# Optimization experiments

Measured on AMD Instinct MI355X. Metric: run time of the kernel, lower is better.

The kernel has to match this reference:

```python
import jax, jax.numpy as jnp
import numpy as np

DIM = 256
HEADS = 4
HEAD_DIM = DIM // HEADS  # 64
SCALE = (DIM / HEADS) ** -0.5
EPS = 1e-5


def layer_norm(x, g, b):
    mu = jnp.mean(x, axis=-1, keepdims=True)
    var = jnp.mean(jnp.square(x - mu), axis=-1, keepdims=True)
    return (x - mu) * jax.lax.rsqrt(var + EPS) * g + b


def setup_inputs() -> dict:
    key = jax.random.key(0)
    ks = jax.random.split(key, 8)
    B, N, C = 2, 64 * 64, DIM
    H = 4 * DIM  # mlp hidden
    s = lambda fan: 1.0 / np.sqrt(fan)
    return {
        "x": jax.random.normal(ks[0], (B, N, C), jnp.float32),
        "w_qkv": jax.random.normal(ks[1], (C, 3 * C), jnp.float32) * s(C),
        "w_ao": jax.random.normal(ks[2], (C, C), jnp.float32) * s(C),
        "b_ao": jnp.zeros((C,), jnp.float32),
        "g_ao": jnp.ones((C,), jnp.float32),
        "be_ao": jnp.zeros((C,), jnp.float32),
        "g1": jnp.ones((C,), jnp.float32),
        "be1": jnp.zeros((C,), jnp.float32),
        "w_fc1": jax.random.normal(ks[3], (C, H), jnp.float32) * s(C),
        "b_fc1": jnp.zeros((H,), jnp.float32),
        "w_fc2": jax.random.normal(ks[4], (H, C), jnp.float32) * s(H),
        "b_fc2": jnp.zeros((C,), jnp.float32),
        "g2": jnp.ones((C,), jnp.float32),
        "be2": jnp.zeros((C,), jnp.float32),
    }


def reference(x, w_qkv, w_ao, b_ao, g_ao, be_ao, g1, be1,
              w_fc1, b_fc1, w_fc2, b_fc2, g2, be2):
    b, n, c = x.shape
    shortcut = x

    # --- LinearAttention ---
    qkv = x @ w_qkv  # [b, n, 3c]
    qkv = qkv.reshape(b, n, 3, HEADS, HEAD_DIM).transpose(2, 0, 3, 1, 4)  # [3,b,h,n,d]
    q, k, v = qkv[0], qkv[1], qkv[2]
    k = jax.nn.softmax(k, axis=-2)  # softmax over sequence dim
    q = q * SCALE
    context = jnp.einsum('bhid,bhjd->bhij', k, v)   # [b,h,n,n]
    out = jnp.einsum('bhij,bhid->bhjd', context, q)  # [b,h,n,d]
    out = out.reshape(b, n, c)  # faithful to torch reshape (no transpose)
    attn_out = layer_norm(out @ w_ao + b_ao, g_ao, be_ao)

    # --- block residuals ---
    h = shortcut + layer_norm(attn_out, g1, be1)
    mlp = jax.nn.gelu(h @ w_fc1 + b_fc1) @ w_fc2 + b_fc2
    h = h + layer_norm(mlp, g2, be2)
    return shortcut + h
```

## Files before the change

kernel.cpp:

```cpp
#include <hip/hip_runtime.h>

typedef __attribute__((ext_vector_type(8))) short short8;
typedef __attribute__((ext_vector_type(4))) float f32x4;

#define EPSF 1e-5f
#define NSEQ 4096
#define R_TOT 8192

__device__ __forceinline__ float bf2f(unsigned short u){
  union { unsigned int i; float f; } v; v.i = ((unsigned int)u) << 16; return v.f;
}
__device__ __forceinline__ unsigned short f2bf(float f){
  union { float f; unsigned int i; } v; v.f = f;
  unsigned int u = v.i;
  u += 0x7FFFu + ((u >> 16) & 1u);
  return (unsigned short)(u >> 16);
}
__device__ __forceinline__ float wsum(float v){
  #pragma unroll
  for (int o = 32; o > 0; o >>= 1) v += __shfl_xor(v, o, 64);
  return v;
}
__device__ __forceinline__ float gelu_tanh(float x){
  float y = 0.7978845608028654f * (x + 0.044715f * x * x * x);
  float e = __expf(2.0f * y);
  float th = 1.0f - 2.0f / (e + 1.0f);
  return 0.5f * x * (1.0f + th);
}
__device__ __forceinline__ void gload_lds16(const unsigned short* g, unsigned short* l){
  __builtin_amdgcn_global_load_lds(
      (const __attribute__((address_space(1))) unsigned int*)g,
      (__attribute__((address_space(3))) unsigned int*)l, 16, 0, 0);
}

__global__ void k_prep(const float* __restrict__ x, unsigned short* __restrict__ xbf,
                       const float* __restrict__ w_qkv, const float* __restrict__ w_ao,
                       const float* __restrict__ w_fc1, const float* __restrict__ w_fc2,
                       unsigned short* __restrict__ oq, unsigned short* __restrict__ oa,
                       unsigned short* __restrict__ o1, unsigned short* __restrict__ o2)
{
  int bid = blockIdx.x;
  const int t = threadIdx.x;
  if (bid < 2048){
    int i = (bid * 256 + t) * 4;
    float4 v = *(const float4*)(x + i);
    ushort4 o;
    o.x = f2bf(v.x); o.y = f2bf(v.y); o.z = f2bf(v.z); o.w = f2bf(v.w);
    *(ushort4*)(xbf + i) = o;
    return;
  }
  bid -= 2048;
  const float* in; unsigned short* out; int rows, cols, tid;
  if (bid < 48)      { in = w_qkv; out = oq; rows = 256;  cols = 768;  tid = bid; }
  else if (bid < 64) { in = w_ao;  out = oa; rows = 256;  cols = 256;  tid = bid - 48; }
  else if (bid < 128){ in = w_fc1; out = o1; rows = 256;  cols = 1024; tid = bid - 64; }
  else               { in = w_fc2; out = o2; rows = 1024; cols = 256;  tid = bid - 128; }
  const int tC = cols >> 6;
  const int r0 = (tid / tC) * 64, c0 = (tid % tC) * 64;
  __shared__ float tile[64][68];
  const int i = t >> 4, j4 = (t & 15) * 4;
  #pragma unroll
  for (int p = 0; p < 4; p++){
    float4 v = *(const float4*)(in + (size_t)(r0 + i + p * 16) * cols + c0 + j4);
    tile[i + p * 16][j4 + 0] = v.x; tile[i + p * 16][j4 + 1] = v.y;
    tile[i + p * 16][j4 + 2] = v.z; tile[i + p * 16][j4 + 3] = v.w;
  }
  __syncthreads();
  #pragma unroll
  for (int p = 0; p < 4; p++){
    int ci = i + p * 16;
    ushort4 o;
    o.x = f2bf(tile[j4 + 0][ci]); o.y = f2bf(tile[j4 + 1][ci]);
    o.z = f2bf(tile[j4 + 2][ci]); o.w = f2bf(tile[j4 + 3][ci]);
    *(ushort4*)(out + (size_t)(c0 + ci) * rows + r0 + j4) = o;
  }
}

template<int BM, int BN, bool HAS_BIAS, bool DO_GELU, bool OUT_BF16>
__global__ __launch_bounds__(256) void k_gemm(const unsigned short* __restrict__ A,
                       const unsigned short* __restrict__ BT,
                       const float* __restrict__ bias,
                       float* __restrict__ Cf,
                       unsigned short* __restrict__ Cb,
                       int M, int N, int K)
{
  constexpr int BK = 64;
  constexpr int FM = BM / 32, FN = BN / 32;
  __shared__ unsigned short As[2][BM * BK];
  __shared__ unsigned short Bs[2][BN * BK];
  const int t  = threadIdx.x;
  const int l  = t & 63;
  const int w  = t >> 6;
  const int wm = w >> 1, wn = w & 1;
  const int lr = l & 15, kq = l >> 4;
  const int m0 = blockIdx.y * BM, n0 = blockIdx.x * BN;

  f32x4 acc[FM][FN];
  #pragma unroll
  for (int i = 0; i < FM; i++)
    #pragma unroll
    for (int j = 0; j < FN; j++) acc[i][j] = (f32x4){0.f, 0.f, 0.f, 0.f};

  const int crow = l >> 3, ccolE = (l & 7) * 8;
  const int nk = K / BK;

  auto stage = [&](int s, int bsel){
    #pragma unroll
    for (int c = w; c < BM / 8; c += 4)
      gload_lds16(A  + (size_t)(m0 + c * 8 + crow) * K + s * BK + ccolE, &As[bsel][c * 512]);
    #pragma unroll
    for (int c = w; c < BN / 8; c += 4)
      gload_lds16(BT + (size_t)(n0 + c * 8 + crow) * K + s * BK + ccolE, &Bs[bsel][c * 512]);
  };

  stage(0, 0);
  __syncthreads();
  for (int s = 0; s < nk; ++s){
    const int cur = s & 1;
    if (s + 1 < nk) stage(s + 1, cur ^ 1);
    #pragma unroll
    for (int kk = 0; kk < BK; kk += 32){
      short8 af[FM], bfr[FN];
      #pragma unroll
      for (int i = 0; i < FM; i++)
        af[i]  = *(const short8*)&As[cur][(wm * (BM / 2) + i * 16 + lr) * 64 + kk + kq * 8];
      #pragma unroll
      for (int j = 0; j < FN; j++)
        bfr[j] = *(const short8*)&Bs[cur][(wn * (BN / 2) + j * 16 + lr) * 64 + kk + kq * 8];
      #pragma unroll
      for (int i = 0; i < FM; i++)
        #pragma unroll
        for (int j = 0; j < FN; j++)
          acc[i][j] = __builtin_amdgcn_mfma_f32_16x16x32_bf16(af[i], bfr[j], acc[i][j], 0, 0, 0);
    }
    __syncthreads();
  }

  const int row0 = m0 + wm * (BM / 2);
  const int col0 = n0 + wn * (BN / 2);
  #pragma unroll
  for (int i = 0; i < FM; i++){
    #pragma unroll
    for (int j = 0; j < FN; j++){
      #pragma unroll
      for (int r = 0; r < 4; r++){
        int row = row0 + i * 16 + kq * 4 + r;
        int col = col0 + j * 16 + lr;
        float v = acc[i][j][r];
        if (HAS_BIAS) v += bias[col];
        if (DO_GELU)  v = gelu_tanh(v);
        if (OUT_BF16) Cb[(size_t)row * N + col] = f2bf(v);
        else          Cf[(size_t)row * N + col] = v;
      }
    }
  }
}

#define NPAD 72
__global__ __launch_bounds__(256) void k_msum(const unsigned short* __restrict__ qkv,
                                              float* __restrict__ Spart,
                                              float* __restrict__ dsum_part)
{
  __shared__ unsigned short kT[64 * NPAD];
  __shared__ unsigned short qT[80 * NPAD];
  const int t = threadIdx.x;
  const int sl = blockIdx.x;
  const int bh = blockIdx.y;
  const int b = bh >> 2, h = bh & 3;
  const int e4 = (t & 15) * 4;
  const int col = (t >> 4) * 4;
  const int w4 = t >> 6, lr = t & 15, kq = (t >> 4) & 3;

  f32x4 acc[5];
  #pragma unroll
  for (int j = 0; j < 5; ++j) acc[j] = (f32x4){0.f, 0.f, 0.f, 0.f};

  for (int ch = 0; ch < 4; ++ch){
    int n = sl * 256 + ch * 64 + col;
    const unsigned short* rp = qkv + (size_t)(b * NSEQ + n) * 768 + h * 64 + e4;
    ushort4 q0 = *(const ushort4*)(rp);
    ushort4 q1 = *(const ushort4*)(rp + 768);
    ushort4 q2 = *(const ushort4*)(rp + 1536);
    ushort4 q3 = *(const ushort4*)(rp + 2304);
    ushort4 k0 = *(const ushort4*)(rp + 256);
    ushort4 k1 = *(const ushort4*)(rp + 1024);
    ushort4 k2 = *(const ushort4*)(rp + 1792);
    ushort4 k3 = *(const ushort4*)(rp + 2560);
    if (ch) __syncthreads();
    ushort4 w;
    w.x = q0.x; w.y = q1.x; w.z = q2.x; w.w = q3.x; *(ushort4*)&qT[(e4+0)*NPAD + col] = w;
    w.x = q0.y; w.y = q1.y; w.z = q2.y; w.w = q3.y; *(ushort4*)&qT[(e4+1)*NPAD + col] = w;
    w.x = q0.z; w.y = q1.z; w.z = q2.z; w.w = q3.z; *(ushort4*)&qT[(e4+2)*NPAD + col] = w;
    w.x = q0.w; w.y = q1.w; w.z = q2.w; w.w = q3.w; *(ushort4*)&qT[(e4+3)*NPAD + col] = w;
    w.x = f2bf(__expf(bf2f(k0.x))); w.y = f2bf(__expf(bf2f(k1.x)));
    w.z = f2bf(__expf(bf2f(k2.x))); w.w = f2bf(__expf(bf2f(k3.x)));
    *(ushort4*)&kT[(e4+0)*NPAD + col] = w;
    w.x = f2bf(__expf(bf2f(k0.y))); w.y = f2bf(__expf(bf2f(k1.y)));
    w.z = f2bf(__expf(bf2f(k2.y))); w.w = f2bf(__expf(bf2f(k3.y)));
    *(ushort4*)&kT[(e4+1)*NPAD + col] = w;
    w.x = f2bf(__expf(bf2f(k0.z))); w.y = f2bf(__expf(bf2f(k1.z)));
    w.z = f2bf(__expf(bf2f(k2.z))); w.w = f2bf(__expf(bf2f(k3.z)));
    *(ushort4*)&kT[(e4+2)*NPAD + col] = w;
    w.x = f2bf(__expf(bf2f(k0.w))); w.y = f2bf(__expf(bf2f(k1.w)));
    w.z = f2bf(__expf(bf2f(k2.w))); w.w = f2bf(__expf(bf2f(k3.w)));
    *(ushort4*)&kT[(e4+3)*NPAD + col] = w;
    if (ch == 0 && t < 16){
      ushort4 ones; ones.x = 0x3F80; ones.y = 0x3F80; ones.z = 0x3F80; ones.w = 0x3F80;
      *(ushort4*)&qT[64 * NPAD + t * 4] = ones;
    }
    __syncthreads();
    #pragma unroll
    for (int ks = 0; ks < 2; ++ks){
      int nc = ks * 32 + kq * 8;
      short8 af = *(const short8*)&kT[(w4 * 16 + lr) * NPAD + nc];
      #pragma unroll
      for (int j = 0; j < 5; ++j){
        short8 bf = *(const short8*)&qT[(j * 16 + lr) * NPAD + nc];
        acc[j] = __builtin_amdgcn_mfma_f32_16x16x32_bf16(af, bf, acc[j], 0, 0, 0);
      }
    }
  }
  float* sp = Spart + ((size_t)sl * 8 + bh) * 4096;
  #pragma unroll
  for (int j = 0; j < 4; ++j)
    #pragma unroll
    for (int r = 0; r < 4; ++r)
      sp[(w4 * 16 + kq * 4 + r) * 64 + j * 16 + lr] = acc[j][r];
  if (lr == 0){
    float* dp = dsum_part + (sl * 8 + bh) * 64;
    #pragma unroll
    for (int r = 0; r < 4; ++r) dp[w4 * 16 + kq * 4 + r] = acc[4][r];
  }
}

__global__ __launch_bounds__(256) void k_projvm_dln(
    const unsigned short* __restrict__ qkv,
    const float* __restrict__ Spart, const float* __restrict__ dsum_part,
    const unsigned short* __restrict__ waoT,
    const float* __restrict__ bias, const float* __restrict__ x,
    const float* __restrict__ g_ao, const float* __restrict__ be_ao,
    const float* __restrict__ g1, const float* __restrict__ be1,
    unsigned short* __restrict__ hbf, float* __restrict__ sxh)
{
  __shared__ __align__(16) char smem[16896 + 16384 + 8192 + 65536];
  unsigned short* As   = (unsigned short*)smem;
  unsigned short* vlds = (unsigned short*)(smem + 16896);
  unsigned short* mt   = (unsigned short*)(smem + 16896 + 16384);
  unsigned short* Bs0  = (unsigned short*)(smem + 41472);
  float*          yt   = (float*)(smem + 41472);

  const int t = threadIdx.x, l = t & 63, w = t >> 6;
  const int lr = l & 15, kq = l >> 4;
  const int m0 = blockIdx.x * 32;
  const int b = m0 >> 12, h = (m0 >> 10) & 3;
  const int bh = b * 4 + h;
  const int n0 = (m0 & 1023) * 4;
  const int crow = l >> 3, ccolE = (l & 7) * 8;

  const unsigned short* vbase = qkv + (size_t)(b * NSEQ + n0) * 768 + 512 + h * 64;
  #pragma unroll
  for (int c = w; c < 16; c += 4)
    gload_lds16(vbase + (size_t)(c * 8 + crow) * 768 + ccolE, vlds + c * 512);
  #pragma unroll
  for (int c = w; c < 32; c += 4)
    gload_lds16(waoT + (size_t)(c * 8 + crow) * 256 + ccolE, Bs0 + c * 512);
  {
    int e = t >> 2, d0 = (t & 3) * 16;
    float dn = 0.f;
    #pragma unroll
    for (int sl = 0; sl < 16; ++sl) dn += dsum_part[(sl * 8 + bh) * 64 + e];
    float rdn = 0.125f / dn;
    #pragma unroll
    for (int i = 0; i < 16; i += 4){
      float4 mv = {0.f, 0.f, 0.f, 0.f};
      #pragma unroll
      for (int sl = 0; sl < 16; ++sl){
        float4 p = *(const float4*)(Spart + ((size_t)sl * 8 + bh) * 4096 + e * 64 + d0 + i);
        mv.x += p.x; mv.y += p.y; mv.z += p.z; mv.w += p.w;
      }
      mt[(d0 + i + 0) * 64 + e] = f2bf(mv.x * rdn);
      mt[(d0 + i + 1) * 64 + e] = f2bf(mv.y * rdn);
      mt[(d0 + i + 2) * 64 + e] = f2bf(mv.z * rdn);
      mt[(d0 + i + 3) * 64 + e] = f2bf(mv.w * rdn);
    }
  }
  __syncthreads();
  {
    f32x4 vacc[2][4];
    #pragma unroll
    for (int i = 0; i < 2; i++)
      #pragma unroll
      for (int j = 0; j < 4; j++) vacc[i][j] = (f32x4){0.f, 0.f, 0.f, 0.f};
    #pragma unroll
    for (int kk = 0; kk < 64; kk += 32){
      short8 vf[2], mf[4];
      #pragma unroll
      for (int i = 0; i < 2; i++)
        vf[i] = *(const short8*)&vlds[((w * 2 + i) * 16 + lr) * 64 + kk + kq * 8];
      #pragma unroll
      for (int j = 0; j < 4; j++)
        mf[j] = *(const short8*)&mt[(j * 16 + lr) * 64 + kk + kq * 8];
      #pragma unroll
      for (int i = 0; i < 2; i++)
        #pragma unroll
        for (int j = 0; j < 4; j++)
          vacc[i][j] = __builtin_amdgcn_mfma_f32_16x16x32_bf16(vf[i], mf[j], vacc[i][j], 0, 0, 0);
    }
    #pragma unroll
    for (int i = 0; i < 2; i++)
      #pragma unroll
      for (int j = 0; j < 4; j++)
        #pragma unroll
        for (int r = 0; r < 4; r++)
          As[((w * 2 + i) * 4 + kq) * 264 + r * 64 + j * 16 + lr] = f2bf(vacc[i][j][r]);
  }
  __syncthreads();
  f32x4 acc[2][4];
  #pragma unroll
  for (int i = 0; i < 2; i++)
    #pragma unroll
    for (int j = 0; j < 4; j++) acc[i][j] = (f32x4){0.f, 0.f, 0.f, 0.f};
  for (int s = 0; s < 4; ++s){
    const int cur = s & 1;
    if (s + 1 < 4){
      unsigned short* bnxt = Bs0 + (cur ^ 1) * 16384;
      #pragma unroll
      for (int c = w; c < 32; c += 4)
        gload_lds16(waoT + (size_t)(c * 8 + crow) * 256 + (s + 1) * 64 + ccolE,
                    bnxt + c * 512);
    }
    const unsigned short* bcur = Bs0 + cur * 16384;
    #pragma unroll
    for (int kk = 0; kk < 64; kk += 32){
      short8 af[2], bfr[4];
      #pragma unroll
      for (int i = 0; i < 2; i++)
        af[i] = *(const short8*)&As[(i * 16 + lr) * 264 + s * 64 + kk + kq * 8];
      #pragma unroll
      for (int j = 0; j < 4; j++)
        bfr[j] = *(const short8*)&bcur[(w * 64 + j * 16 + lr) * 64 + kk + kq * 8];
      #pragma unroll
      for (int i = 0; i < 2; i++)
        #pragma unroll
        for (int j = 0; j < 4; j++)
          acc[i][j] = __builtin_amdgcn_mfma_f32_16x16x32_bf16(af[i], bfr[j], acc[i][j], 0, 0, 0);
    }
    __syncthreads();
  }
  #pragma unroll
  for (int i = 0; i < 2; i++)
    #pragma unroll
    for (int j = 0; j < 4; j++){
      float bv = bias[w * 64 + j * 16 + lr];
      #pragma unroll
      for (int r = 0; r < 4; r++)
        yt[(i * 16 + kq * 4 + r) * 260 + w * 64 + j * 16 + lr] = acc[i][j][r] + bv;
    }
  __syncthreads();
  const int gl = t & 63;
  #pragma unroll
  for (int rp = 0; rp < 8; rp++){
    int row = rp * 4 + (t >> 6);
    float4 v = *(const float4*)(yt + row * 260 + gl * 4);
    float mu = wsum(v.x + v.y + v.z + v.w) * 0.00390625f;
    float dx = v.x - mu, dy = v.y - mu, dz = v.z - mu, dw = v.w - mu;
    float rstd = rsqrtf(wsum(dx*dx + dy*dy + dz*dz + dw*dw) * 0.00390625f + EPSF);
    float4 ga = *(const float4*)(g_ao + gl * 4);
    float4 ba = *(const float4*)(be_ao + gl * 4);
    float zx = dx * rstd * ga.x + ba.x, zy = dy * rstd * ga.y + ba.y;
    float zz = dz * rstd * ga.z + ba.z, zw = dw * rstd * ga.w + ba.w;
    float mu2 = wsum(zx + zy + zz + zw) * 0.00390625f;
    float ex = zx - mu2, ey = zy - mu2, ez = zz - mu2, ew = zw - mu2;
    float rstd2 = rsqrtf(wsum(ex*ex + ey*ey + ez*ez + ew*ew) * 0.00390625f + EPSF);
    float4 gb = *(const float4*)(g1 + gl * 4);
    float4 bb = *(const float4*)(be1 + gl * 4);
    size_t off = (size_t)(m0 + row) * 256 + gl * 4;
    float4 xr = *(const float4*)(x + off);
    float hx = xr.x + ex * rstd2 * gb.x + bb.x;
    float hy = xr.y + ey * rstd2 * gb.y + bb.y;
    float hz = xr.z + ez * rstd2 * gb.z + bb.z;
    float hw = xr.w + ew * rstd2 * gb.w + bb.w;
    ushort4 hb; hb.x = f2bf(hx); hb.y = f2bf(hy); hb.z = f2bf(hz); hb.w = f2bf(hw);
    *(ushort4*)(hbf + off) = hb;
    float4 sv = {xr.x + hx, xr.y + hy, xr.z + hz, xr.w + hw};
    *(float4*)(sxh + off) = sv;
  }
}

__global__ __launch_bounds__(256) void k_fc2_ln(
    const unsigned short* __restrict__ A, const unsigned short* __restrict__ BT,
    const float* __restrict__ bias, const float* __restrict__ sxh,
    const float* __restrict__ g2, const float* __restrict__ be2,
    float* __restrict__ out)
{
  constexpr int K = 1024;
  __shared__ __align__(16) char smem[8192 + 65536];
  unsigned short* As0 = (unsigned short*)smem;
  unsigned short* Bs0 = (unsigned short*)(smem + 8192);
  float* yt = (float*)(smem + 8192);
  const int t = threadIdx.x, l = t & 63, w = t >> 6;
  const int lr = l & 15, kq = l >> 4;
  const int m0 = blockIdx.x * 32;
  const int crow = l >> 3, ccolE = (l & 7) * 8;
  f32x4 acc[2][4];
  #pragma unroll
  for (int i = 0; i < 2; i++)
    #pragma unroll
    for (int j = 0; j < 4; j++) acc[i][j] = (f32x4){0.f, 0.f, 0.f, 0.f};

  auto stage = [&](int s, int bsel){
    gload_lds16(A + (size_t)(m0 + w * 8 + crow) * K + s * 64 + ccolE,
                As0 + bsel * 2048 + w * 512);
    unsigned short* bdst = Bs0 + bsel * 16384;
    #pragma unroll
    for (int c = w; c < 32; c += 4)
      gload_lds16(BT + (size_t)(c * 8 + crow) * K + s * 64 + ccolE, bdst + c * 512);
  };

  stage(0, 0);
  __syncthreads();
  for (int s = 0; s < 16; ++s){
    const int cur = s & 1;
    if (s + 1 < 16) stage(s + 1, cur ^ 1);
    const unsigned short* acur = As0 + cur * 2048;
    const unsigned short* bcur = Bs0 + cur * 16384;
    #pragma unroll
    for (int kk = 0; kk < 64; kk += 32){
      short8 af[2], bfr[4];
      #pragma unroll
      for (int i = 0; i < 2; i++)
        af[i] = *(const short8*)&acur[(i * 16 + lr) * 64 + kk + kq * 8];
      #pragma unroll
      for (int j = 0; j < 4; j++)
        bfr[j] = *(const short8*)&bcur[(w * 64 + j * 16 + lr) * 64 + kk + kq * 8];
      #pragma unroll
      for (int i = 0; i < 2; i++)
        #pragma unroll
        for (int j = 0; j < 4; j++)
          acc[i][j] = __builtin_amdgcn_mfma_f32_16x16x32_bf16(af[i], bfr[j], acc[i][j], 0, 0, 0);
    }
    __syncthreads();
  }
  #pragma unroll
  for (int i = 0; i < 2; i++)
    #pragma unroll
    for (int j = 0; j < 4; j++){
      float bv = bias[w * 64 + j * 16 + lr];
      #pragma unroll
      for (int r = 0; r < 4; r++)
        yt[(i * 16 + kq * 4 + r) * 260 + w * 64 + j * 16 + lr] = acc[i][j][r] + bv;
    }
  __syncthreads();
  const int gl = t & 63;
  #pragma unroll
  for (int rp = 0; rp < 8; rp++){
    int row = rp * 4 + (t >> 6);
    float4 v = *(const float4*)(yt + row * 260 + gl * 4);
    float mu = wsum(v.x + v.y + v.z + v.w) * 0.00390625f;
    float dx = v.x - mu, dy = v.y - mu, dz = v.z - mu, dw = v.w - mu;
    float rstd = rsqrtf(wsum(dx*dx + dy*dy + dz*dz + dw*dw) * 0.00390625f + EPSF);
    float4 g = *(const float4*)(g2 + gl * 4);
    float4 be = *(const float4*)(be2 + gl * 4);
    size_t off = (size_t)(m0 + row) * 256 + gl * 4;
    float4 sv = *(const float4*)(sxh + off);
    float4 o;
    o.x = sv.x + dx * rstd * g.x + be.x;
    o.y = sv.y + dy * rstd * g.y + be.y;
    o.z = sv.z + dz * rstd * g.z + be.z;
    o.w = sv.w + dw * rstd * g.w + be.w;
    *(float4*)(out + off) = o;
  }
}

extern "C" void kernel_launch(void* const* d_in, const int* in_sizes, int n_in,
                              void* d_out, int out_size, void* d_ws, size_t ws_size,
                              hipStream_t stream)
{
  const float* x     = (const float*)d_in[0];
  const float* w_qkv = (const float*)d_in[1];
  const float* w_ao  = (const float*)d_in[2];
  const float* b_ao  = (const float*)d_in[3];
  const float* g_ao  = (const float*)d_in[4];
  const float* be_ao = (const float*)d_in[5];
  const float* g1    = (const float*)d_in[6];
  const float* be1   = (const float*)d_in[7];
  const float* w_fc1 = (const float*)d_in[8];
  const float* b_fc1 = (const float*)d_in[9];
  const float* w_fc2 = (const float*)d_in[10];
  const float* b_fc2 = (const float*)d_in[11];
  const float* g2    = (const float*)d_in[12];
  const float* be2   = (const float*)d_in[13];
  float* out = (float*)d_out;
  char* ws = (char*)d_ws;

  unsigned short* qkv   = (unsigned short*)(ws + 0);
  unsigned short* xbf   = (unsigned short*)(ws + 12582912);
  unsigned short* wqkvT = (unsigned short*)(ws + 16777216);
  unsigned short* waoT  = (unsigned short*)(ws + 17170432);
  unsigned short* wfc1T = (unsigned short*)(ws + 17301504);
  unsigned short* wfc2T = (unsigned short*)(ws + 17825792);
  float* Spart = (float*)(ws + 18350080);
  float* dsum_part = (float*)(ws + 20447232);
  float* sxh   = (float*)(ws + 20480000);
  unsigned short* mlp1 = (unsigned short*)(ws + 28868608);

  k_prep<<<2240, 256, 0, stream>>>(x, xbf, w_qkv, w_ao, w_fc1, w_fc2,
                                   wqkvT, waoT, wfc1T, wfc2T);

  k_gemm<128, 128, false, false, true><<<dim3(6, 64), 256, 0, stream>>>(
      xbf, wqkvT, nullptr, nullptr, qkv, R_TOT, 768, 256);

  k_msum<<<dim3(16, 8), 256, 0, stream>>>(qkv, Spart, dsum_part);

  k_projvm_dln<<<256, 256, 0, stream>>>(qkv, Spart, dsum_part, waoT, b_ao, x,
                                        g_ao, be_ao, g1, be1, xbf, sxh);

  k_gemm<128, 128, true, true, true><<<dim3(8, 64), 256, 0, stream>>>(
      xbf, wfc1T, b_fc1, nullptr, mlp1, R_TOT, 1024, 256);

  k_fc2_ln<<<256, 256, 0, stream>>>(mlp1, wfc2T, b_fc2, sxh, g2, be2, out);
}
```

Measured before the change: 80.54 us.

## Fuse x conversion into QKV GEMM and fc1 GEMM into projection kernel

The x-to-bf16 conversion is dropped from the prep kernel and done inside a dedicated QKV GEMM that loads fp32 x, converts it and writes it to LDS. The fc1 GEMM with GELU is fused into the attention-projection/LayerNorm kernel, so the h tile stays in LDS instead of making a round trip through global memory, and one launch is removed. The k_msum grid is doubled to 32 sequence slices, giving more parallelism but more partials to reduce. The fused kernel uses about 140KB of LDS and runs fc1 on only 256 blocks of 32 rows each, which may limit occupancy.

```diff
diff --git a/kernel.cpp b/kernel.cpp
--- a/kernel.cpp
+++ b/kernel.cpp
@@ -33,23 +33,13 @@
       (__attribute__((address_space(3))) unsigned int*)l, 16, 0, 0);
 }
 
-__global__ void k_prep(const float* __restrict__ x, unsigned short* __restrict__ xbf,
-                       const float* __restrict__ w_qkv, const float* __restrict__ w_ao,
+__global__ void k_prep(const float* __restrict__ w_qkv, const float* __restrict__ w_ao,
                        const float* __restrict__ w_fc1, const float* __restrict__ w_fc2,
                        unsigned short* __restrict__ oq, unsigned short* __restrict__ oa,
                        unsigned short* __restrict__ o1, unsigned short* __restrict__ o2)
 {
   int bid = blockIdx.x;
   const int t = threadIdx.x;
-  if (bid < 2048){
-    int i = (bid * 256 + t) * 4;
-    float4 v = *(const float4*)(x + i);
-    ushort4 o;
-    o.x = f2bf(v.x); o.y = f2bf(v.y); o.z = f2bf(v.z); o.w = f2bf(v.w);
-    *(ushort4*)(xbf + i) = o;
-    return;
-  }
-  bid -= 2048;
   const float* in; unsigned short* out; int rows, cols, tid;
   if (bid < 48)      { in = w_qkv; out = oq; rows = 256;  cols = 768;  tid = bid; }
   else if (bid < 64) { in = w_ao;  out = oa; rows = 256;  cols = 256;  tid = bid - 48; }
@@ -76,84 +66,83 @@
   }
 }
 
-template<int BM, int BN, bool HAS_BIAS, bool DO_GELU, bool OUT_BF16>
-__global__ __launch_bounds__(256) void k_gemm(const unsigned short* __restrict__ A,
-                       const unsigned short* __restrict__ BT,
-                       const float* __restrict__ bias,
-                       float* __restrict__ Cf,
-                       unsigned short* __restrict__ Cb,
-                       int M, int N, int K)
+__global__ __launch_bounds__(256) void k_qkv(const float* __restrict__ X,
+                                             const unsigned short* __restrict__ BT,
+                                             unsigned short* __restrict__ Cb)
 {
-  constexpr int BK = 64;
-  constexpr int FM = BM / 32, FN = BN / 32;
-  __shared__ unsigned short As[2][BM * BK];
-  __shared__ unsigned short Bs[2][BN * BK];
-  const int t  = threadIdx.x;
-  const int l  = t & 63;
-  const int w  = t >> 6;
-  const int wm = w >> 1, wn = w & 1;
-  const int lr = l & 15, kq = l >> 4;
-  const int m0 = blockIdx.y * BM, n0 = blockIdx.x * BN;
-
-  f32x4 acc[FM][FN];
-  #pragma unroll
-  for (int i = 0; i < FM; i++)
-    #pragma unroll
-    for (int j = 0; j < FN; j++) acc[i][j] = (f32x4){0.f, 0.f, 0.f, 0.f};
-
+  constexpr int K = 256, N = 768;
+  __shared__ unsigned short As[2][128 * 72];
+  __shared__ unsigned short Bs[2][128 * 64];
+  const int t = threadIdx.x, l = t & 63, w = t >> 6;
+  const int wm = w >> 1, wn = w & 1, lr = l & 15, kq = l >> 4;
+  const int m0 = blockIdx.y * 128, n0 = blockIdx.x * 128;
+  const int srow = t >> 1, scol = (t & 1) * 32;
   const int crow = l >> 3, ccolE = (l & 7) * 8;
-  const int nk = K / BK;
-
-  auto stage = [&](int s, int bsel){
-    #pragma unroll
-    for (int c = w; c < BM / 8; c += 4)
-      gload_lds16(A  + (size_t)(m0 + c * 8 + crow) * K + s * BK + ccolE, &As[bsel][c * 512]);
-    #pragma unroll
-    for (int c = w; c < BN / 8; c += 4)
-      gload_lds16(BT + (size_t)(n0 + c * 8 + crow) * K + s * BK + ccolE, &Bs[bsel][c * 512]);
+
+  f32x4 acc[4][4];
+  #pragma unroll
+  for (int i = 0; i < 4; i++)
+    #pragma unroll
+    for (int j = 0; j < 4; j++) acc[i][j] = (f32x4){0.f, 0.f, 0.f, 0.f};
+
+  float4 a4[8];
+  auto loadA = [&](int s){
+    const float* xp = X + (size_t)(m0 + srow) * K + s * 64 + scol;
+    #pragma unroll
+    for (int i = 0; i < 8; i++) a4[i] = *(const float4*)(xp + i * 4);
   };
-
-  stage(0, 0);
-  __syncthreads();
-  for (int s = 0; s < nk; ++s){
+  auto writeA = [&](int bsel){
+    unsigned short* d = &As[bsel][srow * 72 + scol];
+    #pragma unroll
+    for (int i = 0; i < 8; i++){
+      ushort4 o;
+      o.x = f2bf(a4[i].x); o.y = f2bf(a4[i].y);
+      o.z = f2bf(a4[i].z); o.w = f2bf(a4[i].w);
+      *(ushort4*)(d + i * 4) = o;
+    }
+  };
+  auto stageB = [&](int s, int bsel){
+    #pragma unroll
+    for (int c = w; c < 16; c += 4)
+      gload_lds16(BT + (size_t)(n0 + c * 8 + crow) * K + s * 64 + ccolE, &Bs[bsel][c * 512]);
+  };
+
+  loadA(0); stageB(0, 0); writeA(0);
+  __syncthreads();
+  for (int s = 0; s < 4; ++s){
     const int cur = s & 1;
-    if (s + 1 < nk) stage(s + 1, cur ^ 1);
-    #pragma unroll
-    for (int kk = 0; kk < BK; kk += 32){
-      short8 af[FM], bfr[FN];
-      #pragma unroll
-      for (int i = 0; i < FM; i++)
-        af[i]  = *(const short8*)&As[cur][(wm * (BM / 2) + i * 16 + lr) * 64 + kk + kq * 8];
-      #pragma unroll
-      for (int j = 0; j < FN; j++)
-        bfr[j] = *(const short8*)&Bs[cur][(wn * (BN / 2) + j * 16 + lr) * 64 + kk + kq * 8];
-      #pragma unroll
-      for (int i = 0; i < FM; i++)
-        #pragma unroll
-        for (int j = 0; j < FN; j++)
+    if (s + 1 < 4){ loadA(s + 1); stageB(s + 1, cur ^ 1); }
+    #pragma unroll
+    for (int kk = 0; kk < 64; kk += 32){
+      short8 af[4], bfr[4];
+      #pragma unroll
+      for (int i = 0; i < 4; i++)
+        af[i]  = *(const short8*)&As[cur][(wm * 64 + i * 16 + lr) * 72 + kk + kq * 8];
+      #pragma unroll
+      for (int j = 0; j < 4; j++)
+        bfr[j] = *(const short8*)&Bs[cur][(wn * 64 + j * 16 + lr) * 64 + kk + kq * 8];
+      #pragma unroll
+      for (int i = 0; i < 4; i++)
+        #pragma unroll
+        for (int j = 0; j < 4; j++)
           acc[i][j] = __builtin_amdgcn_mfma_f32_16x16x32_bf16(af[i], bfr[j], acc[i][j], 0, 0, 0);
     }
+    if (s + 1 < 4) writeA(cur ^ 1);
     __syncthreads();
   }
 
-  const int row0 = m0 + wm * (BM / 2);
-  const int col0 = n0 + wn * (BN / 2);
-  #pragma unroll
-  for (int i = 0; i < FM; i++){
-    #pragma unroll
-    for (int j = 0; j < FN; j++){
+  const int row0 = m0 + wm * 64;
+  const int col0 = n0 + wn * 64;
+  #pragma unroll
+  for (int i = 0; i < 4; i++)
+    #pragma unroll
+    for (int j = 0; j < 4; j++)
       #pragma unroll
       for (int r = 0; r < 4; r++){
         int row = row0 + i * 16 + kq * 4 + r;
         int col = col0 + j * 16 + lr;
-        float v = acc[i][j][r];
-        if (HAS_BIAS) v += bias[col];
-        if (DO_GELU)  v = gelu_tanh(v);
-        if (OUT_BF16) Cb[(size_t)row * N + col] = f2bf(v);
-        else          Cf[(size_t)row * N + col] = v;
+        Cb[(size_t)row * N + col] = f2bf(acc[i][j][r]);
       }
-    }
-  }
 }
 
 #define NPAD 72
@@ -175,8 +164,8 @@
   #pragma unroll
   for (int j = 0; j < 5; ++j) acc[j] = (f32x4){0.f, 0.f, 0.f, 0.f};
 
-  for (int ch = 0; ch < 4; ++ch){
-    int n = sl * 256 + ch * 64 + col;
+  for (int ch = 0; ch < 2; ++ch){
+    int n = sl * 128 + ch * 64 + col;
     const unsigned short* rp = qkv + (size_t)(b * NSEQ + n) * 768 + h * 64 + e4;
     ushort4 q0 = *(const ushort4*)(rp);
     ushort4 q1 = *(const ushort4*)(rp + 768);
@@ -233,21 +222,22 @@
   }
 }
 
-__global__ __launch_bounds__(256) void k_projvm_dln(
+__global__ __launch_bounds__(256) void k_projvm_fc1(
     const unsigned short* __restrict__ qkv,
     const float* __restrict__ Spart, const float* __restrict__ dsum_part,
     const unsigned short* __restrict__ waoT,
     const float* __restrict__ bias, const float* __restrict__ x,
     const float* __restrict__ g_ao, const float* __restrict__ be_ao,
     const float* __restrict__ g1, const float* __restrict__ be1,
-    unsigned short* __restrict__ hbf, float* __restrict__ sxh)
+    const unsigned short* __restrict__ wfc1T, const float* __restrict__ b_fc1,
+    float* __restrict__ sxh, unsigned short* __restrict__ mlp1)
 {
-  __shared__ __align__(16) char smem[16896 + 16384 + 8192 + 65536];
-  unsigned short* As   = (unsigned short*)smem;
+  __shared__ __align__(16) char smem[140288];
+  unsigned short* hA   = (unsigned short*)smem;
   unsigned short* vlds = (unsigned short*)(smem + 16896);
-  unsigned short* mt   = (unsigned short*)(smem + 16896 + 16384);
+  unsigned short* mt   = (unsigned short*)(smem + 33280);
   unsigned short* Bs0  = (unsigned short*)(smem + 41472);
-  float*          yt   = (float*)(smem + 41472);
+  float*          yt   = (float*)(smem + 107008);
 
   const int t = threadIdx.x, l = t & 63, w = t >> 6;
   const int lr = l & 15, kq = l >> 4;
@@ -267,14 +257,14 @@
   {
     int e = t >> 2, d0 = (t & 3) * 16;
     float dn = 0.f;
-    #pragma unroll
-    for (int sl = 0; sl < 16; ++sl) dn += dsum_part[(sl * 8 + bh) * 64 + e];
+    #pragma unroll 8
+    for (int sl = 0; sl < 32; ++sl) dn += dsum_part[(sl * 8 + bh) * 64 + e];
     float rdn = 0.125f / dn;
     #pragma unroll
     for (int i = 0; i < 16; i += 4){
       float4 mv = {0.f, 0.f, 0.f, 0.f};
-      #pragma unroll
-      for (int sl = 0; sl < 16; ++sl){
+      #pragma unroll 8
+      for (int sl = 0; sl < 32; ++sl){
         float4 p = *(const float4*)(Spart + ((size_t)sl * 8 + bh) * 4096 + e * 64 + d0 + i);
         mv.x += p.x; mv.y += p.y; mv.z += p.z; mv.w += p.w;
       }
@@ -312,7 +302,7 @@
       for (int j = 0; j < 4; j++)
         #pragma unroll
         for (int r = 0; r < 4; r++)
-          As[((w * 2 + i) * 4 + kq) * 264 + r * 64 + j * 16 + lr] = f2bf(vacc[i][j][r]);
+          hA[((w * 2 + i) * 4 + kq) * 264 + r * 64 + j * 16 + lr] = f2bf(vacc[i][j][r]);
   }
   __syncthreads();
   f32x4 acc[2][4];
@@ -335,7 +325,7 @@
       short8 af[2], bfr[4];
       #pragma unroll
       for (int i = 0; i < 2; i++)
-        af[i] = *(const short8*)&As[(i * 16 + lr) * 264 + s * 64 + kk + kq * 8];
+        af[i] = *(const short8*)&hA[(i * 16 + lr) * 264 + s * 64 + kk + kq * 8];
       #pragma unroll
       for (int j = 0; j < 4; j++)
         bfr[j] = *(const short8*)&bcur[(w * 64 + j * 16 + lr) * 64 + kk + kq * 8];
@@ -346,6 +336,11 @@
           acc[i][j] = __builtin_amdgcn_mfma_f32_16x16x32_bf16(af[i], bfr[j], acc[i][j], 0, 0, 0);
     }
     __syncthreads();
+  }
+  {
+    #pragma unroll
+    for (int c = w; c < 32; c += 4)
+      gload_lds16(wfc1T + (size_t)(c * 8 + crow) * 256 + ccolE, Bs0 + c * 512);
   }
   #pragma unroll
   for (int i = 0; i < 2; i++)
@@ -381,9 +376,61 @@
     float hz = xr.z + ez * rstd2 * gb.z + bb.z;
     float hw = xr.w + ew * rstd2 * gb.w + bb.w;
     ushort4 hb; hb.x = f2bf(hx); hb.y = f2bf(hy); hb.z = f2bf(hz); hb.w = f2bf(hw);
-    *(ushort4*)(hbf + off) = hb;
+    *(ushort4*)&hA[row * 264 + gl * 4] = hb;
     float4 sv = {xr.x + hx, xr.y + hy, xr.z + hz, xr.w + hw};
     *(float4*)(sxh + off) = sv;
+  }
+  __syncthreads();
+  f32x4 acc1[2][4];
+  #pragma unroll
+  for (int i = 0; i < 2; i++)
+    #pragma unroll
+    for (int j = 0; j < 4; j++) acc1[i][j] = (f32x4){0.f, 0.f, 0.f, 0.f};
+  for (int st = 0; st < 16; ++st){
+    const int cur = st & 1;
+    if (st + 1 < 16){
+      int nch = (st + 1) >> 2, ks = (st + 1) & 3;
+      unsigned short* bnxt = Bs0 + (cur ^ 1) * 16384;
+      #pragma unroll
+      for (int c = w; c < 32; c += 4)
+        gload_lds16(wfc1T + (size_t)(nch * 256 + c * 8 + crow) * 256 + ks * 64 + ccolE,
+                    bnxt + c * 512);
+    }
+    const unsigned short* bcur = Bs0 + cur * 16384;
+    const int ks = st & 3;
+    #pragma unroll
+    for (int kk = 0; kk < 64; kk += 32){
+      short8 af[2], bfr[4];
+      #pragma unroll
+      for (int i = 0; i < 2; i++)
+        af[i] = *(const short8*)&hA[(i * 16 + lr) * 264 + ks * 64 + kk + kq * 8];
+      #pragma unroll
+      for (int j = 0; j < 4; j++)
+        bfr[j] = *(const short8*)&bcur[(w * 64 + j * 16 + lr) * 64 + kk + kq * 8];
+      #pragma unroll
+      for (int i = 0; i < 2; i++)
+        #pragma unroll
+        for (int j = 0; j < 4; j++)
+          acc1[i][j] = __builtin_amdgcn_mfma_f32_16x16x32_bf16(af[i], bfr[j], acc1[i][j], 0, 0, 0);
+    }
+    if (ks == 3){
+      const int nch = st >> 2;
+      #pragma unroll
+      for (int j = 0; j < 4; j++){
+        int col = nch * 256 + w * 64 + j * 16 + lr;
+        float bv = b_fc1[col];
+        #pragma unroll
+        for (int i = 0; i < 2; i++){
+          #pragma unroll
+          for (int r = 0; r < 4; r++){
+            int row = m0 + i * 16 + kq * 4 + r;
+            mlp1[(size_t)row * 1024 + col] = f2bf(gelu_tanh(acc1[i][j][r] + bv));
+          }
+          acc1[i][j] = (f32x4){0.f, 0.f, 0.f, 0.f};
+        }
+      }
+    }
+    __syncthreads();
   }
 }
 
@@ -494,29 +541,25 @@
   char* ws = (char*)d_ws;
 
   unsigned short* qkv   = (unsigned short*)(ws + 0);
-  unsigned short* xbf   = (unsigned short*)(ws + 12582912);
   unsigned short* wqkvT = (unsigned short*)(ws + 16777216);
   unsigned short* waoT  = (unsigned short*)(ws + 17170432);
   unsigned short* wfc1T = (unsigned short*)(ws + 17301504);
   unsigned short* wfc2T = (unsigned short*)(ws + 17825792);
   float* Spart = (float*)(ws + 18350080);
-  float* dsum_part = (float*)(ws + 20447232);
-  float* sxh   = (float*)(ws + 20480000);
-  unsigned short* mlp1 = (unsigned short*)(ws + 28868608);
-
-  k_prep<<<2240, 256, 0, stream>>>(x, xbf, w_qkv, w_ao, w_fc1, w_fc2,
-                                   wqkvT, waoT, wfc1T, wfc2T);
-
-  k_gemm<128, 128, false, false, true><<<dim3(6, 64), 256, 0, stream>>>(
-      xbf, wqkvT, nullptr, nullptr, qkv, R_TOT, 768, 256);
-
-  k_msum<<<dim3(16, 8), 256, 0, stream>>>(qkv, Spart, dsum_part);
-
-  k_projvm_dln<<<256, 256, 0, stream>>>(qkv, Spart, dsum_part, waoT, b_ao, x,
-                                        g_ao, be_ao, g1, be1, xbf, sxh);
-
-  k_gemm<128, 128, true, true, true><<<dim3(8, 64), 256, 0, stream>>>(
-      xbf, wfc1T, b_fc1, nullptr, mlp1, R_TOT, 1024, 256);
+  float* dsum_part = (float*)(ws + 22544384);
+  float* sxh   = (float*)(ws + 22609920);
+  unsigned short* mlp1 = (unsigned short*)(ws + 30998528);
+
+  k_prep<<<192, 256, 0, stream>>>(w_qkv, w_ao, w_fc1, w_fc2,
+                                  wqkvT, waoT, wfc1T, wfc2T);
+
+  k_qkv<<<dim3(6, 64), 256, 0, stream>>>(x, wqkvT, qkv);
+
+  k_msum<<<dim3(32, 8), 256, 0, stream>>>(qkv, Spart, dsum_part);
+
+  k_projvm_fc1<<<256, 256, 0, stream>>>(qkv, Spart, dsum_part, waoT, b_ao, x,
+                                        g_ao, be_ao, g1, be1, wfc1T, b_fc1,
+                                        sxh, mlp1);
 
   k_fc2_ln<<<256, 256, 0, stream>>>(mlp1, wfc2T, b_fc2, sxh, g2, be2, out);
 }
```

Result: slower. 97.11 us (+20.6%).
